# Kernel optimization log

Measured on AMD Instinct MI355X. Metric: run time of the kernel, lower is better.

Reference implementation:

```python
import jax, jax.numpy as jnp
import numpy as np

B, N, C, H, L, WSZ = 4, 16384, 1024, 16, 256, 512
Dh = C // H
Nb = N // B
NW = Nb // WSZ
EPS = 1e-6
SCALE = Dh ** -0.5


def _ln(h, g=None, b=None):
    m = h.mean(-1, keepdims=True)
    v = h.var(-1, keepdims=True)
    h = (h - m) * jax.lax.rsqrt(v + EPS)
    if g is not None:
        h = h * g + b
    return h


def setup_inputs() -> dict:
    key = jax.random.key(0)
    ks = jax.random.split(key, 16)
    s = 0.02
    return {
        'x': jax.random.normal(ks[0], (N, C), jnp.float32),
        'context': jax.random.normal(ks[1], (B, L, C), jnp.float32),
        'mod': jax.random.normal(ks[2], (B, C), jnp.float32),
        'W_mod': jax.random.normal(ks[3], (C, 6 * C), jnp.float32) * s,
        'b_mod': jnp.zeros((6 * C,), jnp.float32),
        'gamma2': jnp.ones((C,), jnp.float32),
        'beta2': jnp.zeros((C,), jnp.float32),
        'W_qkv': jax.random.normal(ks[4], (C, 3 * C), jnp.float32) * s,
        'b_qkv': jnp.zeros((3 * C,), jnp.float32),
        'W_so': jax.random.normal(ks[5], (C, C), jnp.float32) * s,
        'b_so': jnp.zeros((C,), jnp.float32),
        'W_q': jax.random.normal(ks[6], (C, C), jnp.float32) * s,
        'b_q': jnp.zeros((C,), jnp.float32),
        'W_kv': jax.random.normal(ks[7], (C, 2 * C), jnp.float32) * s,
        'b_kv': jnp.zeros((2 * C,), jnp.float32),
        'W_co': jax.random.normal(ks[8], (C, C), jnp.float32) * s,
        'b_co': jnp.zeros((C,), jnp.float32),
        'W_m1': jax.random.normal(ks[9], (C, 4 * C), jnp.float32) * s,
        'b_m1': jnp.zeros((4 * C,), jnp.float32),
        'W_m2': jax.random.normal(ks[10], (4 * C, C), jnp.float32) * s,
        'b_m2': jnp.zeros((C,), jnp.float32),
    }


def reference(x, context, mod, W_mod, b_mod, gamma2, beta2, W_qkv, b_qkv,
              W_so, b_so, W_q, b_q, W_kv, b_kv, W_co, b_co,
              W_m1, b_m1, W_m2, b_m2):
    xb = x.reshape(B, Nb, C)

    # AdaLN modulation: SiLU -> Linear -> 6 chunks, broadcast per batch item
    m6 = jax.nn.silu(mod) @ W_mod + b_mod                   # [B, 6C]
    sh_msa, sc_msa, g_msa, sh_mlp, sc_mlp, g_mlp = jnp.split(m6, 6, axis=-1)

    # --- windowed sparse self-attention ---
    h = _ln(xb) * (1.0 + sc_msa[:, None]) + sh_msa[:, None]
    qkv = (h @ W_qkv + b_qkv).reshape(B, NW, WSZ, 3, H, Dh)
    q, k, v = qkv[:, :, :, 0], qkv[:, :, :, 1], qkv[:, :, :, 2]
    a = jax.nn.softmax(jnp.einsum('bwqhd,bwkhd->bwhqk', q, k) * SCALE, axis=-1)
    o = jnp.einsum('bwhqk,bwkhd->bwqhd', a, v).reshape(B, Nb, C)
    xb = xb + g_msa[:, None] * (o @ W_so + b_so)

    # --- full cross-attention to per-batch context ---
    h = _ln(xb, gamma2, beta2)
    q = (h @ W_q + b_q).reshape(B, Nb, H, Dh)
    kv = (context @ W_kv + b_kv).reshape(B, L, 2, H, Dh)
    k, v = kv[:, :, 0], kv[:, :, 1]
    a = jax.nn.softmax(jnp.einsum('bqhd,bkhd->bhqk', q, k) * SCALE, axis=-1)
    o = jnp.einsum('bhqk,bkhd->bqhd', a, v).reshape(B, Nb, C)
    xb = xb + (o @ W_co + b_co)

    # --- modulated sparse FFN ---
    h = _ln(xb) * (1.0 + sc_mlp[:, None]) + sh_mlp[:, None]
    h = jax.nn.gelu(h @ W_m1 + b_m1, approximate=True)
    xb = xb + g_mlp[:, None] * (h @ W_m2 + b_m2)

    return xb.reshape(N, C)
```

## Files before the change

kernel.cpp:

```cpp
#include <hip/hip_runtime.h>

typedef unsigned short u16;
typedef __attribute__((ext_vector_type(8))) short short8;
typedef __attribute__((ext_vector_type(4))) float f32x4;

#define SCALE_ 0.125f

struct __align__(8) U16x4 { u16 x, y, z, w; };

__device__ __forceinline__ u16 f2b(float f) {
  union { float f; unsigned u; } c; c.f = f;
  unsigned u = c.u;
  u += 0x7fffu + ((u >> 16) & 1u);
  return (u16)(u >> 16);
}

__device__ __forceinline__ void gload16(const void* g, void* l) {
  __builtin_amdgcn_global_load_lds((const __attribute__((address_space(1))) void*)g,
                                   (__attribute__((address_space(3))) void*)l,
                                   16, 0, 0);
}

__device__ __forceinline__ float gelu_t(float x) {
  float z = 1.5957691216057308f * (x + 0.044715f * x * x * x);
  return x / (1.0f + __expf(-z));
}

struct WcastDesc {
  const float* src[8];
  void* dst[8];
  int K[8];
  int N[8];
  int ofs[9];
};

__global__ __launch_bounds__(256) void wcast_all(WcastDesc d) {
  __shared__ float t[32][33];
  const int bid = blockIdx.x;
  int i = 0;
  while (bid >= d.ofs[i + 1]) ++i;
  const int rb = bid - d.ofs[i];
  if (d.K[i] == 0) {
    const int idx = rb * 256 + threadIdx.x;
    const float4 v = ((const float4*)d.src[i])[idx];
    U16x4 o; o.x = f2b(v.x); o.y = f2b(v.y); o.z = f2b(v.z); o.w = f2b(v.w);
    ((U16x4*)d.dst[i])[idx] = o;
    return;
  }
  const float* W = d.src[i];
  u16* Wt = (u16*)d.dst[i];
  const int K = d.K[i], N = d.N[i];
  const int nb = N >> 5;
  const int k0 = (rb / nb) << 5;
  const int n0 = (rb % nb) << 5;
  const int tx = threadIdx.x & 31;
  const int ty = threadIdx.x >> 5;
#pragma unroll
  for (int r = 0; r < 32; r += 8) t[ty + r][tx] = W[(size_t)(k0 + ty + r) * N + n0 + tx];
  __syncthreads();
#pragma unroll
  for (int r = 0; r < 32; r += 8) Wt[(size_t)(n0 + ty + r) * K + k0 + tx] = f2b(t[tx][ty + r]);
}

__global__ __launch_bounds__(256) void mod_gemm(const float* __restrict__ mod,
                                                const float* __restrict__ Wm,
                                                const float* __restrict__ bm,
                                                float* __restrict__ m6) {
  __shared__ float s[4096];
  for (int i = threadIdx.x; i < 4096; i += 256) {
    float x = mod[i];
    s[i] = x / (1.0f + __expf(-x));
  }
  __syncthreads();
  const int j = blockIdx.x * 256 + threadIdx.x;
  float a0 = bm[j], a1 = a0, a2 = a0, a3 = a0;
#pragma unroll 8
  for (int c = 0; c < 1024; c++) {
    float w = Wm[(size_t)c * 6144 + j];
    a0 += s[c] * w;
    a1 += s[1024 + c] * w;
    a2 += s[2048 + c] * w;
    a3 += s[3072 + c] * w;
  }
  m6[j] = a0; m6[6144 + j] = a1; m6[12288 + j] = a2; m6[18432 + j] = a3;
}

__global__ __launch_bounds__(256) void ln_k(const float* __restrict__ x,
                                            u16* __restrict__ out,
                                            const float* __restrict__ g,
                                            const float* __restrict__ bb,
                                            int batch_stride, int add_one) {
  const int row = blockIdx.x;
  const int tid = threadIdx.x;
  const float4 v = ((const float4*)(x + (size_t)row * 1024))[tid];
  float s = v.x + v.y + v.z + v.w;
  float q = v.x * v.x + v.y * v.y + v.z * v.z + v.w * v.w;
#pragma unroll
  for (int m = 1; m < 64; m <<= 1) {
    s += __shfl_xor(s, m, 64);
    q += __shfl_xor(q, m, 64);
  }
  __shared__ float ps[4], pq[4];
  if ((tid & 63) == 0) { ps[tid >> 6] = s; pq[tid >> 6] = q; }
  __syncthreads();
  s = ps[0] + ps[1] + ps[2] + ps[3];
  q = pq[0] + pq[1] + pq[2] + pq[3];
  const float mean = s * (1.0f / 1024.0f);
  const float var = q * (1.0f / 1024.0f) - mean * mean;
  const float rstd = rsqrtf(var + 1e-6f);
  const int batch = row >> 12;
  const float4 gv = ((const float4*)(g + (size_t)batch * batch_stride))[tid];
  const float4 bv = ((const float4*)(bb + (size_t)batch * batch_stride))[tid];
  const float ao = add_one ? 1.0f : 0.0f;
  U16x4 o;
  o.x = f2b((v.x - mean) * rstd * (gv.x + ao) + bv.x);
  o.y = f2b((v.y - mean) * rstd * (gv.y + ao) + bv.y);
  o.z = f2b((v.z - mean) * rstd * (gv.z + ao) + bv.z);
  o.w = f2b((v.w - mean) * rstd * (gv.w + ao) + bv.w);
  ((U16x4*)(out + (size_t)row * 1024))[tid] = o;
}

template <int EPI>
__global__ __launch_bounds__(256) void gemm_bt(const u16* __restrict__ A,
                                               const u16* __restrict__ Bt,
                                               const float* __restrict__ bias,
                                               void* outp, const float* res,
                                               const float* gate, int M, int N,
                                               int K, int gate_stride) {
  __shared__ __align__(16) u16 As[4096];
  __shared__ __align__(16) u16 Bs[4096];
  const int nb = N >> 7;
  const int bm = (blockIdx.x / nb) << 7;
  const int bn = (blockIdx.x % nb) << 7;
  const int tid = threadIdx.x;
  const int lane = tid & 63;
  const int wv = tid >> 6;
  const int wr = (wv >> 1) << 6;
  const int wc = (wv & 1) << 6;
  const int lrow = lane & 15;
  const int lk = lane >> 4;
  const int srow = tid >> 2;
  const int scol = (tid & 3) << 3;
  const u16* gA = A + (size_t)(bm + srow) * K + scol;
  const u16* gB = Bt + (size_t)(bn + srow) * K + scol;
  const size_t rskip = (size_t)64 * K;
  u16* lA = As + wv * 512;
  u16* lB = Bs + wv * 512;
  f32x4 acc[4][4] = {};
  for (int k0 = 0; k0 < K; k0 += 32) {
    gload16(gA + k0, lA);
    gload16(gA + k0 + rskip, lA + 2048);
    gload16(gB + k0, lB);
    gload16(gB + k0 + rskip, lB + 2048);
    __syncthreads();
    short8 a[4], b[4];
#pragma unroll
    for (int m = 0; m < 4; m++)
      a[m] = *(const short8*)(As + (wr + m * 16 + lrow) * 32 + lk * 8);
#pragma unroll
    for (int n = 0; n < 4; n++)
      b[n] = *(const short8*)(Bs + (wc + n * 16 + lrow) * 32 + lk * 8);
#pragma unroll
    for (int m = 0; m < 4; m++)
#pragma unroll
      for (int n = 0; n < 4; n++)
        acc[m][n] = __builtin_amdgcn_mfma_f32_16x16x32_bf16(a[m], b[n], acc[m][n], 0, 0, 0);
    __syncthreads();
  }
#pragma unroll
  for (int m = 0; m < 4; m++) {
    const int row0 = bm + wr + m * 16 + lk * 4;
#pragma unroll
    for (int n = 0; n < 4; n++) {
      const int col = bn + wc + n * 16 + lrow;
      const float bval = bias[col];
#pragma unroll
      for (int j = 0; j < 4; j++) {
        float v = acc[m][n][j] + bval;
        size_t idx = (size_t)(row0 + j) * N + col;
        ((u16*)outp)[idx] = f2b(v);
      }
    }
  }
}

template <int EPI>
__global__ __launch_bounds__(512, 2) void gemm8p(const u16* __restrict__ A,
                                                 const u16* __restrict__ Bt,
                                                 const float* __restrict__ bias,
                                                 void* outp, const float* res,
                                                 const float* gate, int M, int N,
                                                 int K, int gate_stride) {
  extern __shared__ char smem[];
  const int nb = N >> 8;
  const int nwg = (M >> 8) * nb;
  const int cpx = nwg >> 3;
  const int wg = (blockIdx.x & 7) * cpx + (blockIdx.x >> 3);
  const int bm = (wg / nb) << 8;
  const int bn = (wg % nb) << 8;
  const int tid = threadIdx.x;
  const int lane = tid & 63;
  const int w = tid >> 6;
  const int wm = w >> 2;
  const int wn = w & 3;
  const int lrow = lane & 15;
  const int lk = lane >> 4;
  const int u = (lane & 7) ^ (lane >> 3);
  const int r_off = w * 16 + ((lane >> 3) << 1) + (u >> 2);
  const int c_off = (u & 3) << 3;
  const u16* gA = A + (size_t)(bm + r_off) * K + c_off;
  const u16* gB = Bt + (size_t)(bn + r_off) * K + c_off;
  const size_t l_skip = (size_t)128 * K;
  char* sA = smem;
  char* sB = smem + 65536;
  const int dsb = ((lrow >> 1) << 7) + (((((lrow & 1) << 2) + lk) ^ (lrow >> 1)) << 4);
  const int aQ = wm * 8192;
  const int bQ = wn * 4096;

  f32x4 acc[8][4] = {};
  short8 bq[4];
  short8 af[4];

#define SG_A(d, kh, tt)                                                         \
  { gload16(gA + (size_t)(tt) * 64 + (kh) * 32, sA + (d) * 32768 + (kh) * 16384 + w * 1024);            \
    gload16(gA + l_skip + (size_t)(tt) * 64 + (kh) * 32, sA + (d) * 32768 + (kh) * 16384 + (w + 8) * 1024); }
#define SG_B(d, kh, tt)                                                         \
  { gload16(gB + (size_t)(tt) * 64 + (kh) * 32, sB + (d) * 32768 + (kh) * 16384 + w * 1024);            \
    gload16(gB + l_skip + (size_t)(tt) * 64 + (kh) * 32, sB + (d) * 32768 + (kh) * 16384 + (w + 8) * 1024); }
#define RD_A(d, kh, mh)                                                         \
  _Pragma("unroll") for (int m = 0; m < 4; m++)                                 \
    af[m] = *(const short8*)(sA + (d) * 32768 + (kh) * 16384 + aQ + (mh) * 4096 + m * 1024 + dsb);
#define RD_B(d, kh)                                                             \
  _Pragma("unroll") for (int n = 0; n < 4; n++)                                 \
    bq[n] = *(const short8*)(sB + (d) * 32768 + (kh) * 16384 + bQ + n * 1024 + dsb);
#define MM(mh)                                                                  \
  _Pragma("unroll") for (int m = 0; m < 4; m++)                                 \
    _Pragma("unroll") for (int n = 0; n < 4; n++)                               \
      acc[(mh) * 4 + m][n] =                                                    \
          __builtin_amdgcn_mfma_f32_16x16x32_bf16(af[m], bq[n], acc[(mh) * 4 + m][n], 0, 0, 0);
#define SBAR0 __builtin_amdgcn_sched_barrier(0)
#define VM4   asm volatile("s_waitcnt vmcnt(4)" ::: "memory")

  SG_A(0, 0, 0); SG_B(0, 0, 0); SG_A(0, 1, 0); SG_B(0, 1, 0);
  SBAR0;
  VM4;
  __builtin_amdgcn_s_barrier();

  const int nt = K >> 6;
  for (int t = 0; t < nt; ++t) {
    const int d = t & 1;
    const int dn = d ^ 1;
    const int tn = (t + 1 < nt) ? t + 1 : t;
    {
      RD_A(d, 0, 0); RD_B(d, 0);
      SG_A(dn, 0, tn);
      __builtin_amdgcn_s_setprio(1);
      MM(0);
      __builtin_amdgcn_s_setprio(0);
      SBAR0;
    }
    {
      RD_A(d, 0, 1);
      SG_B(dn, 0, tn);
      SBAR0;
      VM4;
      __builtin_amdgcn_s_barrier();
      SBAR0;
      __builtin_amdgcn_s_setprio(1);
      MM(1);
      __builtin_amdgcn_s_setprio(0);
      SBAR0;
    }
    {
      RD_A(d, 1, 0); RD_B(d, 1);
      SG_A(dn, 1, tn);
      __builtin_amdgcn_s_setprio(1);
      MM(0);
      __builtin_amdgcn_s_setprio(0);
      SBAR0;
    }
    {
      RD_A(d, 1, 1);
      SG_B(dn, 1, tn);
      SBAR0;
      VM4;
      __builtin_amdgcn_s_barrier();
      SBAR0;
      __builtin_amdgcn_s_setprio(1);
      MM(1);
      __builtin_amdgcn_s_setprio(0);
      SBAR0;
    }
  }
  asm volatile("s_waitcnt vmcnt(0)" ::: "memory");
#undef SG_A
#undef SG_B
#undef RD_A
#undef RD_B
#undef MM
#undef SBAR0
#undef VM4

  __syncthreads();
  float* eb = (float*)smem + (size_t)w * 1088;
  const float* grow = nullptr;
  if (EPI == 2 && gate) grow = gate + (size_t)(bm >> 12) * gate_stride;
  const int erow = lane >> 4;
  const int ecol = (lane & 15) << 2;
  const int colb = bn + wn * 64 + ecol;
  const float4 bv4 = *(const float4*)(bias + colb);
  float4 gv4 = make_float4(1.0f, 1.0f, 1.0f, 1.0f);
  if (EPI == 2 && grow) gv4 = *(const float4*)(grow + colb);
#pragma unroll
  for (int m = 0; m < 8; m++) {
#pragma unroll
    for (int n = 0; n < 4; n++)
#pragma unroll
      for (int j = 0; j < 4; j++)
        eb[(lk * 4 + j) * 68 + n * 16 + lrow] = acc[m][n][j];
    const int row0 = bm + wm * 128 + m * 16 + erow;
#pragma unroll
    for (int i = 0; i < 4; i++) {
      const int row = row0 + 4 * i;
      float4 v = *(const float4*)(eb + (erow + 4 * i) * 68 + ecol);
      v.x += bv4.x; v.y += bv4.y; v.z += bv4.z; v.w += bv4.w;
      const size_t base = (size_t)row * N + colb;
      if (EPI == 0) {
        U16x4 o; o.x = f2b(v.x); o.y = f2b(v.y); o.z = f2b(v.z); o.w = f2b(v.w);
        *(U16x4*)((u16*)outp + base) = o;
      } else if (EPI == 1) {
        U16x4 o; o.x = f2b(gelu_t(v.x)); o.y = f2b(gelu_t(v.y));
        o.z = f2b(gelu_t(v.z)); o.w = f2b(gelu_t(v.w));
        *(U16x4*)((u16*)outp + base) = o;
      } else {
        const float4 r4 = *(const float4*)(res + base);
        float4 o;
        o.x = r4.x + gv4.x * v.x; o.y = r4.y + gv4.y * v.y;
        o.z = r4.z + gv4.z * v.z; o.w = r4.w + gv4.w * v.w;
        *(float4*)((float*)outp + base) = o;
      }
    }
  }
}

template <int MODE>
__global__ __launch_bounds__(512) void attn_k(const u16* __restrict__ QKV,
                                              const u16* __restrict__ Q2,
                                              const u16* __restrict__ KV2,
                                              u16* __restrict__ O) {
  __shared__ __align__(16) u16 Ks[2][4096];
  __shared__ __align__(16) u16 Vt[2][4096];
  __shared__ __align__(16) u16 Ps[16384];
  const int bid = blockIdx.x;
  const int tid = threadIdx.x;
  const int lane = tid & 63;
  const int wv = tid >> 6;
  const int lrow = lane & 15;
  const int lk = lane >> 4;
  const u16 *qp, *kp, *vp;
  int q_row0, q_stride, kv_row0, kv_stride, nkt, ocol;
  if (MODE == 0) {
    const int qt = bid & 1, h = (bid >> 1) & 15, w = (bid >> 5) & 7, b = bid >> 8;
    const int win = (b * 8 + w) * 512;
    q_row0 = win + qt * 256; q_stride = 3072;
    qp = QKV + h * 64;
    kp = QKV + 1024 + h * 64;
    vp = QKV + 2048 + h * 64;
    kv_row0 = win; kv_stride = 3072; nkt = 8;
    ocol = h * 64;
  } else {
    const int qt = bid & 15, h = (bid >> 4) & 15, b = bid >> 8;
    q_row0 = b * 4096 + qt * 256; q_stride = 1024;
    qp = Q2 + h * 64;
    kp = KV2 + h * 64;
    vp = KV2 + 1024 + h * 64;
    kv_row0 = b * 256; kv_stride = 2048; nkt = 4;
    ocol = h * 64;
  }
  const int qr = q_row0 + wv * 32;
  short8 qf[2][2];
#pragma unroll
  for (int m = 0; m < 2; m++)
#pragma unroll
    for (int kk = 0; kk < 2; kk++)
      qf[m][kk] = *(const short8*)(qp + (size_t)(qr + m * 16 + lrow) * q_stride + kk * 32 + lk * 8);
  f32x4 oa[2][4] = {};
  float lst[2][4];
#pragma unroll
  for (int m = 0; m < 2; m++)
#pragma unroll
    for (int j = 0; j < 4; j++) lst[m][j] = 0.0f;

  const int srow = tid >> 3;
  const int schk = tid & 7;
  {
    gload16(kp + (size_t)(kv_row0 + srow) * kv_stride + ((schk ^ (srow & 7)) << 3),
            Ks[0] + wv * 512);
    short8 vv = *(const short8*)(vp + (size_t)(kv_row0 + srow) * kv_stride + (schk << 3));
#pragma unroll
    for (int i = 0; i < 8; i++) {
      const int ii = (i + schk) & 7;
      const int dd = (schk << 3) + ii;
      Vt[0][dd * 64 + (((srow >> 3) ^ (dd & 7)) << 3) + (srow & 7)] = (u16)vv[ii];
    }
  }
  __syncthreads();

  u16* Pw = Ps + wv * 2048;
  for (int kt = 0; kt < nkt; kt++) {
    const int cur = kt & 1, nxt = cur ^ 1;
    const int have = (kt + 1 < nkt);
    short8 vv;
    if (have) {
      const int kvr1 = kv_row0 + (kt + 1) * 64;
      gload16(kp + (size_t)(kvr1 + srow) * kv_stride + ((schk ^ (srow & 7)) << 3),
              Ks[nxt] + wv * 512);
      vv = *(const short8*)(vp + (size_t)(kvr1 + srow) * kv_stride + (schk << 3));
    }
    f32x4 s[2][4] = {};
    __builtin_amdgcn_s_setprio(1);
#pragma unroll
    for (int n = 0; n < 4; n++)
#pragma unroll
      for (int kk = 0; kk < 2; kk++) {
        short8 kb = *(const short8*)(Ks[cur] + (n * 16 + lrow) * 64 + (((kk * 4 + lk) ^ (lrow & 7)) << 3));
        s[0][n] = __builtin_amdgcn_mfma_f32_16x16x32_bf16(qf[0][kk], kb, s[0][n], 0, 0, 0);
        s[1][n] = __builtin_amdgcn_mfma_f32_16x16x32_bf16(qf[1][kk], kb, s[1][n], 0, 0, 0);
      }
    __builtin_amdgcn_s_setprio(0);
    if (have) {
#pragma unroll
      for (int i = 0; i < 8; i++) {
        const int ii = (i + schk) & 7;
        const int dd = (schk << 3) + ii;
        Vt[nxt][dd * 64 + (((srow >> 3) ^ (dd & 7)) << 3) + (srow & 7)] = (u16)vv[ii];
      }
    }
#pragma unroll
    for (int m = 0; m < 2; m++)
#pragma unroll
      for (int j = 0; j < 4; j++) {
        const float p0 = __expf(s[m][0][j] * SCALE_);
        const float p1 = __expf(s[m][1][j] * SCALE_);
        const float p2 = __expf(s[m][2][j] * SCALE_);
        const float p3 = __expf(s[m][3][j] * SCALE_);
        lst[m][j] += p0 + p1 + p2 + p3;
        const int prow = m * 16 + lk * 4 + j;
        const int base = prow * 64;
        const int r7 = prow & 7;
        const int kl = lrow >> 3, k7 = lrow & 7;
        Pw[base + (((0 + kl) ^ r7) << 3) + k7] = f2b(p0);
        Pw[base + (((2 + kl) ^ r7) << 3) + k7] = f2b(p1);
        Pw[base + (((4 + kl) ^ r7) << 3) + k7] = f2b(p2);
        Pw[base + (((6 + kl) ^ r7) << 3) + k7] = f2b(p3);
      }
#pragma unroll
    for (int kk = 0; kk < 2; kk++) {
      const int sw = ((kk * 4 + lk) ^ (lrow & 7)) << 3;
      short8 pa0 = *(const short8*)(Pw + lrow * 64 + sw);
      short8 pa1 = *(const short8*)(Pw + (16 + lrow) * 64 + sw);
      __builtin_amdgcn_s_setprio(1);
#pragma unroll
      for (int dn = 0; dn < 4; dn++) {
        short8 vb = *(const short8*)(Vt[cur] + (dn * 16 + lrow) * 64 + sw);
        oa[0][dn] = __builtin_amdgcn_mfma_f32_16x16x32_bf16(pa0, vb, oa[0][dn], 0, 0, 0);
        oa[1][dn] = __builtin_amdgcn_mfma_f32_16x16x32_bf16(pa1, vb, oa[1][dn], 0, 0, 0);
      }
      __builtin_amdgcn_s_setprio(0);
    }
    __syncthreads();
  }
#pragma unroll
  for (int m = 0; m < 2; m++)
#pragma unroll
    for (int j = 0; j < 4; j++) {
      float rs = lst[m][j];
      rs += __shfl_xor(rs, 1, 64);
      rs += __shfl_xor(rs, 2, 64);
      rs += __shfl_xor(rs, 4, 64);
      rs += __shfl_xor(rs, 8, 64);
      const float inv = 1.0f / rs;
      const int orow = qr + m * 16 + lk * 4 + j;
#pragma unroll
      for (int dn = 0; dn < 4; dn++)
        O[(size_t)orow * 1024 + ocol + dn * 16 + lrow] = f2b(oa[m][dn][j] * inv);
    }
}

extern "C" void kernel_launch(void* const* d_in, const int* in_sizes, int n_in,
                              void* d_out, int out_size, void* d_ws, size_t ws_size,
                              hipStream_t stream) {
  (void)in_sizes; (void)n_in; (void)out_size; (void)ws_size;
  const float* x      = (const float*)d_in[0];
  const float* ctx    = (const float*)d_in[1];
  const float* mod    = (const float*)d_in[2];
  const float* W_mod  = (const float*)d_in[3];
  const float* b_mod  = (const float*)d_in[4];
  const float* gamma2 = (const float*)d_in[5];
  const float* beta2  = (const float*)d_in[6];
  const float* W_qkv  = (const float*)d_in[7];
  const float* b_qkv  = (const float*)d_in[8];
  const float* W_so   = (const float*)d_in[9];
  const float* b_so   = (const float*)d_in[10];
  const float* W_q    = (const float*)d_in[11];
  const float* b_q    = (const float*)d_in[12];
  const float* W_kv   = (const float*)d_in[13];
  const float* b_kv   = (const float*)d_in[14];
  const float* W_co   = (const float*)d_in[15];
  const float* b_co   = (const float*)d_in[16];
  const float* W_m1   = (const float*)d_in[17];
  const float* b_m1   = (const float*)d_in[18];
  const float* W_m2   = (const float*)d_in[19];
  const float* b_m2   = (const float*)d_in[20];

  char* ws = (char*)d_ws;
  u16*   wt_qkv = (u16*)(ws + 0);
  u16*   wt_so  = (u16*)(ws + 6291456);
  u16*   wt_q   = (u16*)(ws + 8388608);
  u16*   wt_kv  = (u16*)(ws + 10485760);
  u16*   wt_co  = (u16*)(ws + 14680064);
  u16*   wt_m1  = (u16*)(ws + 16777216);
  u16*   wt_m2  = (u16*)(ws + 25165824);
  float* m6     = (float*)(ws + 33554432);
  u16*   ctxb   = (u16*)(ws + 33652736);
  u16*   kvb    = (u16*)(ws + 35749888);
  u16*   bufH   = (u16*)(ws + 39944192);
  u16*   bufO   = (u16*)(ws + 73498624);
  u16*   bufA   = (u16*)(ws + 107053056);
  float* xb1    = (float*)(ws + 107053056 + 50331648);
  float* outp   = (float*)d_out;

  hipFuncSetAttribute(reinterpret_cast<const void*>(&gemm8p<0>),
                      hipFuncAttributeMaxDynamicSharedMemorySize, 131072);
  hipFuncSetAttribute(reinterpret_cast<const void*>(&gemm8p<1>),
                      hipFuncAttributeMaxDynamicSharedMemorySize, 131072);
  hipFuncSetAttribute(reinterpret_cast<const void*>(&gemm8p<2>),
                      hipFuncAttributeMaxDynamicSharedMemorySize, 131072);

  WcastDesc wd;
  wd.src[0] = W_qkv; wd.dst[0] = wt_qkv; wd.K[0] = 1024; wd.N[0] = 3072;
  wd.src[1] = W_so;  wd.dst[1] = wt_so;  wd.K[1] = 1024; wd.N[1] = 1024;
  wd.src[2] = W_q;   wd.dst[2] = wt_q;   wd.K[2] = 1024; wd.N[2] = 1024;
  wd.src[3] = W_kv;  wd.dst[3] = wt_kv;  wd.K[3] = 1024; wd.N[3] = 2048;
  wd.src[4] = W_co;  wd.dst[4] = wt_co;  wd.K[4] = 1024; wd.N[4] = 1024;
  wd.src[5] = W_m1;  wd.dst[5] = wt_m1;  wd.K[5] = 1024; wd.N[5] = 4096;
  wd.src[6] = W_m2;  wd.dst[6] = wt_m2;  wd.K[6] = 4096; wd.N[6] = 1024;
  wd.src[7] = ctx;   wd.dst[7] = ctxb;   wd.K[7] = 0;    wd.N[7] = 0;
  wd.ofs[0] = 0;     wd.ofs[1] = 3072;  wd.ofs[2] = 4096; wd.ofs[3] = 5120;
  wd.ofs[4] = 7168;  wd.ofs[5] = 8192;  wd.ofs[6] = 12288; wd.ofs[7] = 16384;
  wd.ofs[8] = 17408;
  wcast_all<<<17408, 256, 0, stream>>>(wd);

  mod_gemm<<<24, 256, 0, stream>>>(mod, W_mod, b_mod, m6);

  ln_k<<<16384, 256, 0, stream>>>(x, bufH, m6 + 1024, m6 + 0, 6144, 1);
  gemm8p<0><<<768, 512, 131072, stream>>>(bufH, wt_qkv, b_qkv, bufA, nullptr, nullptr, 16384, 3072, 1024, 0);
  attn_k<0><<<1024, 512, 0, stream>>>(bufA, nullptr, nullptr, bufO);
  gemm8p<2><<<256, 512, 131072, stream>>>(bufO, wt_so, b_so, xb1, x, m6 + 2048, 16384, 1024, 1024, 6144);

  ln_k<<<16384, 256, 0, stream>>>(xb1, bufH, gamma2, beta2, 0, 0);
  gemm8p<0><<<256, 512, 131072, stream>>>(bufH, wt_q, b_q, bufA, nullptr, nullptr, 16384, 1024, 1024, 0);
  gemm_bt<0><<<128, 256, 0, stream>>>(ctxb, wt_kv, b_kv, kvb, nullptr, nullptr, 1024, 2048, 1024, 0);
  attn_k<1><<<1024, 512, 0, stream>>>(nullptr, bufA, kvb, bufO);
  gemm8p<2><<<256, 512, 131072, stream>>>(bufO, wt_co, b_co, outp, xb1, nullptr, 16384, 1024, 1024, 0);

  ln_k<<<16384, 256, 0, stream>>>(outp, bufH, m6 + 4096, m6 + 3072, 6144, 1);
  gemm8p<1><<<1024, 512, 131072, stream>>>(bufH, wt_m1, b_m1, bufA, nullptr, nullptr, 16384, 4096, 1024, 0);
  gemm8p<2><<<256, 512, 131072, stream>>>(bufA, wt_m2, b_m2, outp, outp, m6 + 5120, 16384, 1024, 4096, 6144);
}
```

Baseline: 896.2 us.

## Double-buffer LDS fragment registers and interleave ds_reads with MFMAs in GEMM loop

The GEMM main loop now keeps two register sets for the A and B fragments and prefetches the next sub-tile's LDS reads while the current MFMA block runs. sched_group_barrier hints interleave ds_read and MFMA instructions so that LDS latency hides behind matrix math, replacing the previous read-then-compute sequence. This raises VGPR pressure, which could lower occupancy or cause spills. The last phase prefetches from the next buffer, so the cross-iteration ordering depends on the barriers already in the loop.

```diff
diff --git a/kernel.cpp b/kernel.cpp
--- a/kernel.cpp
+++ b/kernel.cpp
@@ -218,8 +218,7 @@
   const int bQ = wn * 4096;
 
   f32x4 acc[8][4] = {};
-  short8 bq[4];
-  short8 af[4];
+  short8 af0[4], af1[4], bq0[4], bq1[4];
 
 #define SG_A(d, kh, tt)                                                         \
   { gload16(gA + (size_t)(tt) * 64 + (kh) * 32, sA + (d) * 32768 + (kh) * 16384 + w * 1024);            \
@@ -227,17 +226,24 @@
 #define SG_B(d, kh, tt)                                                         \
   { gload16(gB + (size_t)(tt) * 64 + (kh) * 32, sB + (d) * 32768 + (kh) * 16384 + w * 1024);            \
     gload16(gB + l_skip + (size_t)(tt) * 64 + (kh) * 32, sB + (d) * 32768 + (kh) * 16384 + (w + 8) * 1024); }
-#define RD_A(d, kh, mh)                                                         \
+#define RD_AF(buf, d, kh, mh)                                                   \
   _Pragma("unroll") for (int m = 0; m < 4; m++)                                 \
-    af[m] = *(const short8*)(sA + (d) * 32768 + (kh) * 16384 + aQ + (mh) * 4096 + m * 1024 + dsb);
-#define RD_B(d, kh)                                                             \
+    buf[m] = *(const short8*)(sA + (d) * 32768 + (kh) * 16384 + aQ + (mh) * 4096 + m * 1024 + dsb);
+#define RD_BQ(buf, d, kh)                                                       \
   _Pragma("unroll") for (int n = 0; n < 4; n++)                                 \
-    bq[n] = *(const short8*)(sB + (d) * 32768 + (kh) * 16384 + bQ + n * 1024 + dsb);
-#define MM(mh)                                                                  \
+    buf[n] = *(const short8*)(sB + (d) * 32768 + (kh) * 16384 + bQ + n * 1024 + dsb);
+#define MM(mh, abuf, bbuf)                                                      \
+  __builtin_amdgcn_s_setprio(1);                                                \
   _Pragma("unroll") for (int m = 0; m < 4; m++)                                 \
     _Pragma("unroll") for (int n = 0; n < 4; n++)                               \
       acc[(mh) * 4 + m][n] =                                                    \
-          __builtin_amdgcn_mfma_f32_16x16x32_bf16(af[m], bq[n], acc[(mh) * 4 + m][n], 0, 0, 0);
+          __builtin_amdgcn_mfma_f32_16x16x32_bf16(abuf[m], bbuf[n], acc[(mh) * 4 + m][n], 0, 0, 0); \
+  __builtin_amdgcn_s_setprio(0);
+#define ILV(NR)                                                                 \
+  _Pragma("unroll") for (int gq = 0; gq < 4; gq++) {                            \
+    __builtin_amdgcn_sched_group_barrier(0x100, (NR), 0);                       \
+    __builtin_amdgcn_sched_group_barrier(0x8, 4, 0);                            \
+  }
 #define SBAR0 __builtin_amdgcn_sched_barrier(0)
 #define VM4   asm volatile("s_waitcnt vmcnt(4)" ::: "memory")
 
@@ -245,6 +251,8 @@
   SBAR0;
   VM4;
   __builtin_amdgcn_s_barrier();
+  SBAR0;
+  RD_AF(af0, 0, 0, 0); RD_BQ(bq0, 0, 0);
 
   const int nt = K >> 6;
   for (int t = 0; t < nt; ++t) {
@@ -252,52 +260,47 @@
     const int dn = d ^ 1;
     const int tn = (t + 1 < nt) ? t + 1 : t;
     {
-      RD_A(d, 0, 0); RD_B(d, 0);
+      RD_AF(af1, d, 0, 1);
       SG_A(dn, 0, tn);
-      __builtin_amdgcn_s_setprio(1);
-      MM(0);
-      __builtin_amdgcn_s_setprio(0);
-      SBAR0;
+      __builtin_amdgcn_sched_group_barrier(0x20, 2, 0);
+      MM(0, af0, bq0);
+      ILV(1);
     }
     {
-      RD_A(d, 0, 1);
       SG_B(dn, 0, tn);
       SBAR0;
       VM4;
       __builtin_amdgcn_s_barrier();
       SBAR0;
-      __builtin_amdgcn_s_setprio(1);
-      MM(1);
-      __builtin_amdgcn_s_setprio(0);
-      SBAR0;
+      RD_AF(af0, d, 1, 0); RD_BQ(bq1, d, 1);
+      MM(1, af1, bq0);
+      ILV(2);
     }
     {
-      RD_A(d, 1, 0); RD_B(d, 1);
+      RD_AF(af1, d, 1, 1);
       SG_A(dn, 1, tn);
-      __builtin_amdgcn_s_setprio(1);
-      MM(0);
-      __builtin_amdgcn_s_setprio(0);
-      SBAR0;
+      __builtin_amdgcn_sched_group_barrier(0x20, 2, 0);
+      MM(0, af0, bq1);
+      ILV(1);
     }
     {
-      RD_A(d, 1, 1);
       SG_B(dn, 1, tn);
       SBAR0;
       VM4;
       __builtin_amdgcn_s_barrier();
       SBAR0;
-      __builtin_amdgcn_s_setprio(1);
-      MM(1);
-      __builtin_amdgcn_s_setprio(0);
-      SBAR0;
+      RD_AF(af0, dn, 0, 0); RD_BQ(bq0, dn, 0);
+      MM(1, af1, bq1);
+      ILV(2);
     }
   }
   asm volatile("s_waitcnt vmcnt(0)" ::: "memory");
 #undef SG_A
 #undef SG_B
-#undef RD_A
-#undef RD_B
+#undef RD_AF
+#undef RD_BQ
 #undef MM
+#undef ILV
 #undef SBAR0
 #undef VM4
 
```

Result: no change. 913.8 us (+2.0%).

## Restructure GEMM main loop into quadrant-based 8-wave ping-pong schedule

Applied to the files above, without the earlier changes.

Rewrites the 256x256 bf16 GEMM mainloop. Shared memory becomes a full 64-wide K tile per row with an XOR chunk swizzle, and the loop is split into four MFMA quadrant phases separated by workgroup barriers, in the style of the HipKittens 8-wave ping-pong schedule. Each wave now keeps A/B fragments for both K halves and reuses B fragments across two M quadrants. The aim is to overlap global-to-LDS loads with MFMA work more evenly and to cut LDS read traffic. In exchange it adds more barriers per iteration, a full vmcnt(0) wait each tile, and higher register pressure.

```diff
diff --git a/kernel.cpp b/kernel.cpp
--- a/kernel.cpp
+++ b/kernel.cpp
@@ -205,46 +205,51 @@
   const int wn = w & 3;
   const int lrow = lane & 15;
   const int lk = lane >> 4;
-  const int u = (lane & 7) ^ (lane >> 3);
-  const int r_off = w * 16 + ((lane >> 3) << 1) + (u >> 2);
-  const int c_off = (u & 3) << 3;
-  const u16* gA = A + (size_t)(bm + r_off) * K + c_off;
-  const u16* gB = Bt + (size_t)(bn + r_off) * K + c_off;
-  const size_t l_skip = (size_t)128 * K;
-  char* sA = smem;
-  char* sB = smem + 65536;
-  const int dsb = ((lrow >> 1) << 7) + (((((lrow & 1) << 2) + lk) ^ (lrow >> 1)) << 4);
-  const int aQ = wm * 8192;
-  const int bQ = wn * 4096;
+  const int tr = tid >> 3;
+  const int chunkS = (tid & 7) ^ (tr & 7);
+  const u16* gAr = A + (size_t)(bm + tr) * K + chunkS * 8;
+  const u16* gBr = Bt + (size_t)(bn + tr) * K + chunkS * 8;
+  const int sk0 = ((lk) ^ (lrow & 7)) << 4;
+  const int sk1 = ((4 + lk) ^ (lrow & 7)) << 4;
+  const int dsA = wm * 16384 + lrow * 128;
+  const int dsB = 32768 + (wn >> 1) * 16384 + ((wn & 1) * 64 + lrow) * 128;
 
   f32x4 acc[8][4] = {};
-  short8 bq[4];
-  short8 af[4];
-
-#define SG_A(d, kh, tt)                                                         \
-  { gload16(gA + (size_t)(tt) * 64 + (kh) * 32, sA + (d) * 32768 + (kh) * 16384 + w * 1024);            \
-    gload16(gA + l_skip + (size_t)(tt) * 64 + (kh) * 32, sA + (d) * 32768 + (kh) * 16384 + (w + 8) * 1024); }
-#define SG_B(d, kh, tt)                                                         \
-  { gload16(gB + (size_t)(tt) * 64 + (kh) * 32, sB + (d) * 32768 + (kh) * 16384 + w * 1024);            \
-    gload16(gB + l_skip + (size_t)(tt) * 64 + (kh) * 32, sB + (d) * 32768 + (kh) * 16384 + (w + 8) * 1024); }
-#define RD_A(d, kh, mh)                                                         \
-  _Pragma("unroll") for (int m = 0; m < 4; m++)                                 \
-    af[m] = *(const short8*)(sA + (d) * 32768 + (kh) * 16384 + aQ + (mh) * 4096 + m * 1024 + dsb);
-#define RD_B(d, kh)                                                             \
-  _Pragma("unroll") for (int n = 0; n < 4; n++)                                 \
-    bq[n] = *(const short8*)(sB + (d) * 32768 + (kh) * 16384 + bQ + n * 1024 + dsb);
-#define MM(mh)                                                                  \
-  _Pragma("unroll") for (int m = 0; m < 4; m++)                                 \
-    _Pragma("unroll") for (int n = 0; n < 4; n++)                               \
-      acc[(mh) * 4 + m][n] =                                                    \
-          __builtin_amdgcn_mfma_f32_16x16x32_bf16(af[m], bq[n], acc[(mh) * 4 + m][n], 0, 0, 0);
+  short8 af[4][2];
+  short8 bq[2][2][2];
+
+#define SG_A(d, h, tt)                                                          \
+  { gload16(gAr + (size_t)((h) * 128) * K + (tt) * 64, smem + (d) * 65536 + (h) * 16384 + tid * 16);        \
+    gload16(gAr + (size_t)((h) * 128 + 64) * K + (tt) * 64, smem + (d) * 65536 + (h) * 16384 + 8192 + tid * 16); }
+#define SG_B(d, h, tt)                                                          \
+  { gload16(gBr + (size_t)((h) * 128) * K + (tt) * 64, smem + (d) * 65536 + 32768 + (h) * 16384 + tid * 16); \
+    gload16(gBr + (size_t)((h) * 128 + 64) * K + (tt) * 64, smem + (d) * 65536 + 32768 + (h) * 16384 + 8192 + tid * 16); }
+#define RD_A(d, mq)                                                             \
+  _Pragma("unroll") for (int f = 0; f < 4; f++) {                               \
+    af[f][0] = *(const short8*)(smem + (d) * 65536 + dsA + ((mq) * 64 + f * 16) * 128 + sk0); \
+    af[f][1] = *(const short8*)(smem + (d) * 65536 + dsA + ((mq) * 64 + f * 16) * 128 + sk1); \
+  }
+#define RD_B(d, nq)                                                             \
+  _Pragma("unroll") for (int f2 = 0; f2 < 2; f2++) {                            \
+    bq[nq][f2][0] = *(const short8*)(smem + (d) * 65536 + dsB + ((nq) * 32 + f2 * 16) * 128 + sk0); \
+    bq[nq][f2][1] = *(const short8*)(smem + (d) * 65536 + dsB + ((nq) * 32 + f2 * 16) * 128 + sk1); \
+  }
+#define MM(mq, nq)                                                              \
+  __builtin_amdgcn_s_setprio(1);                                                \
+  _Pragma("unroll") for (int f = 0; f < 4; f++)                                 \
+    _Pragma("unroll") for (int f2 = 0; f2 < 2; f2++)                            \
+      _Pragma("unroll") for (int kk = 0; kk < 2; kk++)                          \
+        acc[(mq) * 4 + f][(nq) * 2 + f2] = __builtin_amdgcn_mfma_f32_16x16x32_bf16( \
+            af[f][kk], bq[nq][f2][kk], acc[(mq) * 4 + f][(nq) * 2 + f2], 0, 0, 0);  \
+  __builtin_amdgcn_s_setprio(0);
 #define SBAR0 __builtin_amdgcn_sched_barrier(0)
-#define VM4   asm volatile("s_waitcnt vmcnt(4)" ::: "memory")
+#define BAR   __builtin_amdgcn_s_barrier()
+#define VM0   asm volatile("s_waitcnt vmcnt(0)" ::: "memory")
 
   SG_A(0, 0, 0); SG_B(0, 0, 0); SG_A(0, 1, 0); SG_B(0, 1, 0);
   SBAR0;
-  VM4;
-  __builtin_amdgcn_s_barrier();
+  VM0;
+  BAR;
 
   const int nt = K >> 6;
   for (int t = 0; t < nt; ++t) {
@@ -252,54 +257,42 @@
     const int dn = d ^ 1;
     const int tn = (t + 1 < nt) ? t + 1 : t;
     {
-      RD_A(d, 0, 0); RD_B(d, 0);
-      SG_A(dn, 0, tn);
-      __builtin_amdgcn_s_setprio(1);
-      MM(0);
-      __builtin_amdgcn_s_setprio(0);
+      RD_A(d, 0); RD_B(d, 0);
+      SG_A(dn, 0, tn); SG_B(dn, 0, tn);
+      SBAR0; BAR; SBAR0;
+      MM(0, 0);
+      SBAR0; BAR;
+    }
+    {
+      RD_B(d, 1);
+      SG_A(dn, 1, tn); SG_B(dn, 1, tn);
+      SBAR0; BAR; SBAR0;
+      MM(0, 1);
+      SBAR0; BAR;
+    }
+    {
+      RD_A(d, 1);
+      SBAR0; BAR; SBAR0;
+      MM(1, 1);
+      SBAR0; BAR;
+    }
+    {
       SBAR0;
-    }
-    {
-      RD_A(d, 0, 1);
-      SG_B(dn, 0, tn);
-      SBAR0;
-      VM4;
-      __builtin_amdgcn_s_barrier();
-      SBAR0;
-      __builtin_amdgcn_s_setprio(1);
-      MM(1);
-      __builtin_amdgcn_s_setprio(0);
-      SBAR0;
-    }
-    {
-      RD_A(d, 1, 0); RD_B(d, 1);
-      SG_A(dn, 1, tn);
-      __builtin_amdgcn_s_setprio(1);
-      MM(0);
-      __builtin_amdgcn_s_setprio(0);
-      SBAR0;
-    }
-    {
-      RD_A(d, 1, 1);
-      SG_B(dn, 1, tn);
-      SBAR0;
-      VM4;
-      __builtin_amdgcn_s_barrier();
-      SBAR0;
-      __builtin_amdgcn_s_setprio(1);
-      MM(1);
-      __builtin_amdgcn_s_setprio(0);
-      SBAR0;
-    }
-  }
-  asm volatile("s_waitcnt vmcnt(0)" ::: "memory");
+      VM0;
+      BAR; SBAR0;
+      MM(1, 0);
+      SBAR0; BAR;
+    }
+  }
+  VM0;
 #undef SG_A
 #undef SG_B
 #undef RD_A
 #undef RD_B
 #undef MM
 #undef SBAR0
-#undef VM4
+#undef BAR
+#undef VM0
 
   __syncthreads();
   float* eb = (float*)smem + (size_t)w * 1088;
```

After: 915.9 us. 1.02x slower.
